# Kernel tuning notes

Hardware: AMD Instinct MI355X
Metric: run time of the kernel (lower is better)

Reference implementation:

```python
import jax, jax.numpy as jnp
import numpy as np

N = 10000      # nodes
E = 320000     # edges (avg degree 32)
D_IN = 128     # input feature dim
D_H = 256      # hidden dim
L = 3          # num GIN layers


def setup_inputs() -> dict:
    key = jax.random.key(0)
    ks = jax.random.split(key, 2 + 4 * L)
    inp = {
        "x": jax.random.normal(ks[0], (N, D_IN), dtype=jnp.float32),
        "edge_index": jax.random.randint(ks[1], (2, E), 0, N, dtype=jnp.int64),
    }
    din = D_IN
    for l in range(L):
        k1, k2, k3, k4 = ks[2 + 4 * l: 6 + 4 * l]
        s1 = 1.0 / np.sqrt(din)
        s2 = 1.0 / np.sqrt(D_H)
        inp[f"w1_{l}"] = jax.random.uniform(k1, (din, D_H), jnp.float32, -s1, s1)
        inp[f"b1_{l}"] = jax.random.uniform(k2, (D_H,), jnp.float32, -s1, s1)
        inp[f"w2_{l}"] = jax.random.uniform(k3, (D_H, D_H), jnp.float32, -s2, s2)
        inp[f"b2_{l}"] = jax.random.uniform(k4, (D_H,), jnp.float32, -s2, s2)
        din = D_H
    return inp


def reference(x, edge_index,
              w1_0, b1_0, w2_0, b2_0,
              w1_1, b1_1, w2_1, b2_1,
              w1_2, b1_2, w2_2, b2_2):
    src, dst = edge_index[0], edge_index[1]
    layers = [(w1_0, b1_0, w2_0, b2_0),
              (w1_1, b1_1, w2_1, b2_1),
              (w1_2, b1_2, w2_2, b2_2)]
    z = x
    for w1, b1, w2, b2 in layers:
        # GINConv with eps=0: h_i = z_i + sum_{j->i} z_j, then 2-layer MLP
        agg = jax.ops.segment_sum(z[src], dst, num_segments=N)  # [N, d]
        h = z + agg
        h = jax.nn.relu(h @ w1 + b1) @ w2 + b2  # nn.Sequential(Linear, ReLU, Linear)
        z = jax.nn.relu(h)                      # Encoder activation
    return z
```

## Files before the change

kernel.cpp:

```cpp
#include <hip/hip_runtime.h>
#include <hip/hip_bf16.h>
#include <cstdint>


#define NNODES 10000
#define NEDGES 320000
#define DIN 128
#define DH 256

typedef __bf16 bf16x8 __attribute__((ext_vector_type(8)));
typedef unsigned short ushort8v __attribute__((ext_vector_type(8)));
typedef unsigned short ushort4v __attribute__((ext_vector_type(4)));
typedef float f32x4 __attribute__((ext_vector_type(4)));

__device__ __forceinline__ unsigned short f2bf(float f) {
    unsigned int u = __float_as_uint(f);
    unsigned int r = u + 0x7fffu + ((u >> 16) & 1u);
    return (unsigned short)(r >> 16);
}
__device__ __forceinline__ float bf2f(unsigned short u) {
    return __uint_as_float(((unsigned int)u) << 16);
}

struct PrepArgs {
    const float* wsrc[6];
    unsigned short* wdst[6];
    int wkbits[6];
    const int* eb;
    int* flag;
    int* cnt;
    const float* x;
    unsigned short* xb;
};
#define PREP_ZERO_B 40
#define PREP_XCONV_B 1250
#define PREP_WCONV_B 352
#define PREP_GRID (PREP_ZERO_B + 1 + PREP_XCONV_B + PREP_WCONV_B)

__global__ void prep_kernel(PrepArgs a) {
    __shared__ float tile[32][33];
    __shared__ int any;
    int bid = blockIdx.x;
    int tid = threadIdx.x;
    if (bid < PREP_ZERO_B) {
        int i = bid * 256 + tid;
        if (i < NNODES) a.cnt[i] = 0;
    } else if (bid == PREP_ZERO_B) {
        if (tid == 0) any = 0;
        __syncthreads();
        for (int i = tid; i < 1024; i += 256)
            if (a.eb[2 * i + 1] != 0) any = 1;
        __syncthreads();
        if (tid == 0) a.flag[0] = any;
    } else if (bid < PREP_ZERO_B + 1 + PREP_XCONV_B) {
        int i = (bid - PREP_ZERO_B - 1) * 256 + tid;
        if (i < NNODES * DIN / 4) {
            float4 v = reinterpret_cast<const float4*>(a.x)[i];
            ushort4v o = {f2bf(v.x), f2bf(v.y), f2bf(v.z), f2bf(v.w)};
            reinterpret_cast<ushort4v*>(a.xb)[i] = o;
        }
    } else {
        int wb = bid - (PREP_ZERO_B + 1 + PREP_XCONV_B);
        int m, t32;
        if (wb < 32) { m = 0; t32 = wb; }
        else { m = 1 + (wb - 32) / 64; t32 = (wb - 32) % 64; }
        int kb = a.wkbits[m];
        int K = 1 << kb;
        int tc = t32 & 7, tr = t32 >> 3;
        int r = tid >> 3, c4 = (tid & 7) * 4;
        float4 v = *reinterpret_cast<const float4*>(
            &a.wsrc[m][(size_t)(tr * 32 + r) * 256 + tc * 32 + c4]);
        tile[r][c4 + 0] = v.x; tile[r][c4 + 1] = v.y;
        tile[r][c4 + 2] = v.z; tile[r][c4 + 3] = v.w;
        __syncthreads();
        int cc = tid >> 3, k4 = (tid & 7) * 4;
        ushort4v o = {f2bf(tile[k4 + 0][cc]), f2bf(tile[k4 + 1][cc]),
                      f2bf(tile[k4 + 2][cc]), f2bf(tile[k4 + 3][cc])};
        *reinterpret_cast<ushort4v*>(
            &a.wdst[m][(size_t)(tc * 32 + cc) * K + tr * 32 + k4]) = o;
    }
}

__device__ __forceinline__ int eload(const int* __restrict__ eb, int is32, long logical_idx) {
    return is32 ? eb[logical_idx] : eb[2 * logical_idx];
}

__global__ void hist_kernel(const int* __restrict__ eb, const int* __restrict__ flag,
                            int* __restrict__ cnt, int E) {
    int i = blockIdx.x * blockDim.x + threadIdx.x;
    if (i >= E) return;
    int is32 = flag[0];
    int d = eload(eb, is32, (long)E + i);
    atomicAdd(&cnt[d], 1);
}

__global__ __launch_bounds__(1024) void scan_kernel(const int* __restrict__ cnt,
                                                    int* __restrict__ offs,
                                                    int* __restrict__ cursor, int n) {
    __shared__ int wsums[16];
    int tid = threadIdx.x, lane = tid & 63, wid = tid >> 6;
    int per = (n + 1023) / 1024;
    int beg = tid * per;
    int local[16];
    int s = 0;
    for (int i = 0; i < per; ++i) {
        int idx = beg + i;
        int v = (idx < n) ? cnt[idx] : 0;
        local[i] = s;
        s += v;
    }
    int inc = s;
    for (int d = 1; d < 64; d <<= 1) {
        int y = __shfl_up(inc, d, 64);
        if (lane >= d) inc += y;
    }
    if (lane == 63) wsums[wid] = inc;
    __syncthreads();
    if (tid < 16) {
        int v = wsums[tid];
        for (int d = 1; d < 16; d <<= 1) {
            int y = __shfl_up(v, d, 64);
            if (tid >= d) v += y;
        }
        wsums[tid] = v;
    }
    __syncthreads();
    int wbase = (wid > 0) ? wsums[wid - 1] : 0;
    int base = wbase + inc - s;
    for (int i = 0; i < per; ++i) {
        int idx = beg + i;
        if (idx < n) {
            int v = base + local[i];
            offs[idx] = v;
            cursor[idx] = v;
        }
    }
    if (tid == 1023) offs[n] = wbase + inc;
}

__global__ void scatter_kernel(const int* __restrict__ eb, const int* __restrict__ flag,
                               int* __restrict__ cursor, int* __restrict__ srcs, int E) {
    int i = blockIdx.x * blockDim.x + threadIdx.x;
    if (i >= E) return;
    int is32 = flag[0];
    int s = eload(eb, is32, (long)i);
    int d = eload(eb, is32, (long)E + i);
    int pos = atomicAdd(&cursor[d], 1);
    srcs[pos] = s;
}

template <int D>
__global__ __launch_bounds__(256) void agg_add_sliced_kernel(const unsigned short* __restrict__ z,
                                                             const int* __restrict__ srcs,
                                                             const int* __restrict__ offs,
                                                             unsigned short* __restrict__ h, int n) {
    constexpr int NSLICE = (D * 2) / 128;
    constexpr int LPN = 8;
    constexpr int NPB = 256 / LPN;
    int bid = blockIdx.x;
    int slice = bid & (NSLICE - 1);
    int ng = bid / NSLICE;
    int t = threadIdx.x;
    int node = ng * NPB + t / LPN;
    if (node >= n) return;
    int li = t % LPN;
    int col8 = slice * LPN + li;
    const ushort8v* zb = reinterpret_cast<const ushort8v*>(z);
    const int ld8 = D / 8;
    int beg = offs[node], end = offs[node + 1];

    float a0[8] = {}, a1[8] = {}, a2[8] = {}, a3[8] = {};
    int e = beg;
    for (; e + 4 <= end; e += 4) {
        int s0 = srcs[e], s1 = srcs[e + 1], s2 = srcs[e + 2], s3 = srcs[e + 3];
        ushort8v v0 = zb[(size_t)s0 * ld8 + col8];
        ushort8v v1 = zb[(size_t)s1 * ld8 + col8];
        ushort8v v2 = zb[(size_t)s2 * ld8 + col8];
        ushort8v v3 = zb[(size_t)s3 * ld8 + col8];
#pragma unroll
        for (int j = 0; j < 8; ++j) {
            a0[j] += bf2f(v0[j]);
            a1[j] += bf2f(v1[j]);
            a2[j] += bf2f(v2[j]);
            a3[j] += bf2f(v3[j]);
        }
    }
    for (; e < end; ++e) {
        ushort8v v = zb[(size_t)srcs[e] * ld8 + col8];
#pragma unroll
        for (int j = 0; j < 8; ++j) a0[j] += bf2f(v[j]);
    }
    ushort8v zr = zb[(size_t)node * ld8 + col8];
    ushort8v o;
#pragma unroll
    for (int j = 0; j < 8; ++j) {
        float v = a0[j] + a1[j] + a2[j] + a3[j] + bf2f(zr[j]);
        o[j] = f2bf(v);
    }
    reinterpret_cast<ushort8v*>(h)[(size_t)node * ld8 + col8] = o;
}

template <int K, int OUT_BF16>
__global__ __launch_bounds__(512) void mlp_fused_kernel(const unsigned short* __restrict__ A,
                                                        const unsigned short* __restrict__ Wt1,
                                                        const float* __restrict__ b1,
                                                        const unsigned short* __restrict__ Wt2,
                                                        const float* __restrict__ b2,
                                                        void* __restrict__ C, int M) {
    constexpr int NK = K / 32;
    constexpr int NST1 = K / 128;
    __shared__ unsigned short As[NK][4][64][8];
    __shared__ unsigned short Bs[4][4][256][8];
    __shared__ unsigned short Ts[8][4][64][8];
    int tid = threadIdx.x;
    int wave = tid >> 6, lane = tid & 63;
    int wr = wave >> 2, wc = wave & 3;
    int m0 = blockIdx.x * 64;
    int fr = lane & 15;
    int kc = lane >> 4;

    f32x4 acc[2][4];
#pragma unroll
    for (int i = 0; i < 2; ++i)
#pragma unroll
        for (int j = 0; j < 4; ++j) acc[i][j] = (f32x4){0.f, 0.f, 0.f, 0.f};

    {
        int row = tid >> 3, c0 = tid & 7;
        int gr = m0 + row;
#pragma unroll
        for (int i = 0; i < K / 64; ++i) {
            int chunk = c0 + i * 8;
            ushort8v av = {0, 0, 0, 0, 0, 0, 0, 0};
            if (gr < M) av = *reinterpret_cast<const ushort8v*>(&A[(size_t)gr * K + chunk * 8]);
            *reinterpret_cast<ushort8v*>(&As[chunk >> 2][chunk & 3][row][0]) = av;
        }
    }
    int scol = tid >> 2;
    int sscn = tid & 3;

#pragma unroll
    for (int st = 0; st < NST1; ++st) {
#pragma unroll
        for (int cp = 0; cp < 2; ++cp) {
            int c = cp * 128 + scol;
#pragma unroll
            for (int kk = 0; kk < 4; ++kk)
                *reinterpret_cast<ushort8v*>(&Bs[kk][sscn][c][0]) =
                    *reinterpret_cast<const ushort8v*>(&Wt1[(size_t)c * K + st * 128 + kk * 32 + sscn * 8]);
        }
        __syncthreads();
#pragma unroll
        for (int kk = 0; kk < 4; ++kk) {
            bf16x8 af[2];
#pragma unroll
            for (int i = 0; i < 2; ++i)
                af[i] = __builtin_bit_cast(bf16x8,
                    *reinterpret_cast<const ushort8v*>(&As[st * 4 + kk][kc][wr * 32 + i * 16 + fr][0]));
#pragma unroll
            for (int j = 0; j < 4; ++j) {
                bf16x8 bf = __builtin_bit_cast(bf16x8,
                    *reinterpret_cast<const ushort8v*>(&Bs[kk][kc][wc * 64 + j * 16 + fr][0]));
#pragma unroll
                for (int i = 0; i < 2; ++i)
                    acc[i][j] = __builtin_amdgcn_mfma_f32_16x16x32_bf16(af[i], bf, acc[i][j], 0, 0, 0);
            }
        }
        __syncthreads();
    }
#pragma unroll
    for (int i = 0; i < 2; ++i)
#pragma unroll
        for (int j = 0; j < 4; ++j) {
            int col = wc * 64 + j * 16 + fr;
            float bb = b1[col];
#pragma unroll
            for (int jj = 0; jj < 4; ++jj) {
                int row = wr * 32 + i * 16 + kc * 4 + jj;
                float v = fmaxf(acc[i][j][jj] + bb, 0.f);
                Ts[col >> 5][(col >> 3) & 3][row][col & 7] = f2bf(v);
            }
            acc[i][j] = (f32x4){0.f, 0.f, 0.f, 0.f};
        }

#pragma unroll
    for (int st = 0; st < 2; ++st) {
#pragma unroll
        for (int cp = 0; cp < 2; ++cp) {
            int c = cp * 128 + scol;
#pragma unroll
            for (int kk = 0; kk < 4; ++kk)
                *reinterpret_cast<ushort8v*>(&Bs[kk][sscn][c][0]) =
                    *reinterpret_cast<const ushort8v*>(&Wt2[(size_t)c * 256 + st * 128 + kk * 32 + sscn * 8]);
        }
        __syncthreads();
#pragma unroll
        for (int kk = 0; kk < 4; ++kk) {
            bf16x8 af[2];
#pragma unroll
            for (int i = 0; i < 2; ++i)
                af[i] = __builtin_bit_cast(bf16x8,
                    *reinterpret_cast<const ushort8v*>(&Ts[st * 4 + kk][kc][wr * 32 + i * 16 + fr][0]));
#pragma unroll
            for (int j = 0; j < 4; ++j) {
                bf16x8 bf = __builtin_bit_cast(bf16x8,
                    *reinterpret_cast<const ushort8v*>(&Bs[kk][kc][wc * 64 + j * 16 + fr][0]));
#pragma unroll
                for (int i = 0; i < 2; ++i)
                    acc[i][j] = __builtin_amdgcn_mfma_f32_16x16x32_bf16(af[i], bf, acc[i][j], 0, 0, 0);
            }
        }
        __syncthreads();
    }
#pragma unroll
    for (int i = 0; i < 2; ++i)
#pragma unroll
        for (int j = 0; j < 4; ++j) {
            int col = wc * 64 + j * 16 + fr;
            float bb = b2[col];
#pragma unroll
            for (int jj = 0; jj < 4; ++jj) {
                int row = m0 + wr * 32 + i * 16 + kc * 4 + jj;
                if (row < M) {
                    float v = fmaxf(acc[i][j][jj] + bb, 0.f);
                    if (OUT_BF16)
                        ((unsigned short*)C)[(size_t)row * 256 + col] = f2bf(v);
                    else
                        ((float*)C)[(size_t)row * 256 + col] = v;
                }
            }
        }
}

extern "C" void kernel_launch(void* const* d_in, const int* in_sizes, int n_in,
                              void* d_out, int out_size, void* d_ws, size_t ws_size,
                              hipStream_t stream) {
    const float* x = (const float*)d_in[0];
    const int* eb = (const int*)d_in[1];
    const int E = NEDGES;
    const int N = NNODES;

    const float* w1[3] = {(const float*)d_in[2], (const float*)d_in[6], (const float*)d_in[10]};
    const float* b1[3] = {(const float*)d_in[3], (const float*)d_in[7], (const float*)d_in[11]};
    const float* w2[3] = {(const float*)d_in[4], (const float*)d_in[8], (const float*)d_in[12]};
    const float* b2[3] = {(const float*)d_in[5], (const float*)d_in[9], (const float*)d_in[13]};

    char* ws = (char*)d_ws;
    size_t off = 0;
    auto alloc = [&](size_t bytes) {
        void* p = ws + off;
        off += (bytes + 255) & ~(size_t)255;
        return p;
    };
    int* flag   = (int*)alloc(4);
    int* cnt    = (int*)alloc((size_t)N * 4);
    int* offs   = (int*)alloc((size_t)(N + 1) * 4);
    int* cursor = (int*)alloc((size_t)N * 4);
    int* srcs   = (int*)alloc((size_t)E * 4);
    unsigned short* xb   = (unsigned short*)alloc((size_t)N * DIN * 2);
    unsigned short* zbuf = (unsigned short*)alloc((size_t)N * DH * 2);
    unsigned short* hbuf = (unsigned short*)alloc((size_t)N * DH * 2);
    unsigned short* wt[6];
    wt[0] = (unsigned short*)alloc((size_t)DIN * DH * 2);
    for (int i = 1; i < 6; ++i) wt[i] = (unsigned short*)alloc((size_t)DH * DH * 2);
    (void)ws_size; (void)n_in; (void)out_size; (void)in_sizes;

    PrepArgs pa;
    pa.wsrc[0] = w1[0]; pa.wsrc[1] = w2[0]; pa.wsrc[2] = w1[1];
    pa.wsrc[3] = w2[1]; pa.wsrc[4] = w1[2]; pa.wsrc[5] = w2[2];
    for (int i = 0; i < 6; ++i) pa.wdst[i] = wt[i];
    pa.wkbits[0] = 7;
    for (int i = 1; i < 6; ++i) pa.wkbits[i] = 8;
    pa.eb = eb; pa.flag = flag; pa.cnt = cnt; pa.x = x; pa.xb = xb;
    prep_kernel<<<PREP_GRID, 256, 0, stream>>>(pa);

    hist_kernel<<<(E + 255) / 256, 256, 0, stream>>>(eb, flag, cnt, E);
    scan_kernel<<<1, 1024, 0, stream>>>(cnt, offs, cursor, N);
    scatter_kernel<<<(E + 255) / 256, 256, 0, stream>>>(eb, flag, cursor, srcs, E);

    int mlp_grid = (N + 63) / 64;
    int agg_blocks_256 = ((N + 31) / 32) * 4;
    int agg_blocks_128 = ((N + 31) / 32) * 2;

    agg_add_sliced_kernel<128><<<agg_blocks_128, 256, 0, stream>>>(xb, srcs, offs, hbuf, N);
    mlp_fused_kernel<128, 1><<<mlp_grid, 512, 0, stream>>>(hbuf, wt[0], b1[0], wt[1], b2[0], zbuf, N);

    agg_add_sliced_kernel<256><<<agg_blocks_256, 256, 0, stream>>>(zbuf, srcs, offs, hbuf, N);
    mlp_fused_kernel<256, 1><<<mlp_grid, 512, 0, stream>>>(hbuf, wt[2], b1[1], wt[3], b2[1], zbuf, N);

    agg_add_sliced_kernel<256><<<agg_blocks_256, 256, 0, stream>>>(zbuf, srcs, offs, hbuf, N);
    mlp_fused_kernel<256, 0><<<mlp_grid, 512, 0, stream>>>(hbuf, wt[4], b1[2], wt[5], b2[2], (float*)d_out, N);
}
```

Baseline: 146.7 us.

## Prefetch next weight tile into registers while computing current stage in fused MLP

Restructures the fused two-layer MLP kernel so the next 128-wide weight slab is loaded from global memory into registers while MFMAs run on the current slab in shared memory. Each register slab is written to shared memory after a barrier. This software pipelining is meant to hide global weight-load latency behind compute. It costs 8 extra 16-byte vector registers per thread, which may affect occupancy, and it adds a more intricate barrier schedule.

New measurement: 146.7 us. Within noise of the previous version (-0.0%).

```diff
diff --git a/kernel.cpp b/kernel.cpp
--- a/kernel.cpp
+++ b/kernel.cpp
@@ -218,6 +218,8 @@
     int m0 = blockIdx.x * 64;
     int fr = lane & 15;
     int kc = lane >> 4;
+    int scol = tid >> 2;
+    int sscn = tid & 3;
 
     f32x4 acc[2][4];
 #pragma unroll
@@ -225,6 +227,83 @@
 #pragma unroll
         for (int j = 0; j < 4; ++j) acc[i][j] = (f32x4){0.f, 0.f, 0.f, 0.f};
 
+    ushort8v wreg[8];
+#define LOAD_W(Wp, ldk, st)                                                   \
+    {                                                                         \
+        _Pragma("unroll")                                                     \
+        for (int cp = 0; cp < 2; ++cp) {                                      \
+            _Pragma("unroll")                                                 \
+            for (int kk = 0; kk < 4; ++kk)                                    \
+                wreg[cp * 4 + kk] = *reinterpret_cast<const ushort8v*>(       \
+                    &(Wp)[(size_t)(cp * 128 + scol) * (ldk) + (st) * 128 +    \
+                          kk * 32 + sscn * 8]);                               \
+        }                                                                     \
+    }
+#define WRITE_W()                                                             \
+    {                                                                         \
+        _Pragma("unroll")                                                     \
+        for (int cp = 0; cp < 2; ++cp) {                                      \
+            _Pragma("unroll")                                                 \
+            for (int kk = 0; kk < 4; ++kk)                                    \
+                *reinterpret_cast<ushort8v*>(                                 \
+                    &Bs[kk][sscn][cp * 128 + scol][0]) = wreg[cp * 4 + kk];   \
+        }                                                                     \
+    }
+
+    auto compute_p1 = [&](int st) {
+#pragma unroll
+        for (int kk = 0; kk < 4; ++kk) {
+            bf16x8 af[2];
+#pragma unroll
+            for (int i = 0; i < 2; ++i)
+                af[i] = __builtin_bit_cast(bf16x8,
+                    *reinterpret_cast<const ushort8v*>(&As[st * 4 + kk][kc][wr * 32 + i * 16 + fr][0]));
+#pragma unroll
+            for (int j = 0; j < 4; ++j) {
+                bf16x8 bf = __builtin_bit_cast(bf16x8,
+                    *reinterpret_cast<const ushort8v*>(&Bs[kk][kc][wc * 64 + j * 16 + fr][0]));
+#pragma unroll
+                for (int i = 0; i < 2; ++i)
+                    acc[i][j] = __builtin_amdgcn_mfma_f32_16x16x32_bf16(af[i], bf, acc[i][j], 0, 0, 0);
+            }
+        }
+    };
+    auto compute_p2 = [&](int st) {
+#pragma unroll
+        for (int kk = 0; kk < 4; ++kk) {
+            bf16x8 af[2];
+#pragma unroll
+            for (int i = 0; i < 2; ++i)
+                af[i] = __builtin_bit_cast(bf16x8,
+                    *reinterpret_cast<const ushort8v*>(&Ts[st * 4 + kk][kc][wr * 32 + i * 16 + fr][0]));
+#pragma unroll
+            for (int j = 0; j < 4; ++j) {
+                bf16x8 bf = __builtin_bit_cast(bf16x8,
+                    *reinterpret_cast<const ushort8v*>(&Bs[kk][kc][wc * 64 + j * 16 + fr][0]));
+#pragma unroll
+                for (int i = 0; i < 2; ++i)
+                    acc[i][j] = __builtin_amdgcn_mfma_f32_16x16x32_bf16(af[i], bf, acc[i][j], 0, 0, 0);
+            }
+        }
+    };
+    auto epilogue1 = [&]() {
+#pragma unroll
+        for (int i = 0; i < 2; ++i)
+#pragma unroll
+            for (int j = 0; j < 4; ++j) {
+                int col = wc * 64 + j * 16 + fr;
+                float bb = b1[col];
+#pragma unroll
+                for (int jj = 0; jj < 4; ++jj) {
+                    int row = wr * 32 + i * 16 + kc * 4 + jj;
+                    float v = fmaxf(acc[i][j][jj] + bb, 0.f);
+                    Ts[col >> 5][(col >> 3) & 3][row][col & 7] = f2bf(v);
+                }
+                acc[i][j] = (f32x4){0.f, 0.f, 0.f, 0.f};
+            }
+    };
+
+    LOAD_W(Wt1, K, 0);
     {
         int row = tid >> 3, c0 = tid & 7;
         int gr = m0 + row;
@@ -236,82 +315,29 @@
             *reinterpret_cast<ushort8v*>(&As[chunk >> 2][chunk & 3][row][0]) = av;
         }
     }
-    int scol = tid >> 2;
-    int sscn = tid & 3;
-
-#pragma unroll
-    for (int st = 0; st < NST1; ++st) {
-#pragma unroll
-        for (int cp = 0; cp < 2; ++cp) {
-            int c = cp * 128 + scol;
-#pragma unroll
-            for (int kk = 0; kk < 4; ++kk)
-                *reinterpret_cast<ushort8v*>(&Bs[kk][sscn][c][0]) =
-                    *reinterpret_cast<const ushort8v*>(&Wt1[(size_t)c * K + st * 128 + kk * 32 + sscn * 8]);
-        }
+    WRITE_W();
+    if (NST1 > 1) { LOAD_W(Wt1, K, 1); } else { LOAD_W(Wt2, 256, 0); }
+    __syncthreads();
+    compute_p1(0);
+    if (NST1 == 1) epilogue1();
+    __syncthreads();
+    WRITE_W();
+    if (NST1 > 1) { LOAD_W(Wt2, 256, 0); } else { LOAD_W(Wt2, 256, 1); }
+    __syncthreads();
+    if (NST1 > 1) {
+        compute_p1(1);
+        epilogue1();
         __syncthreads();
-#pragma unroll
-        for (int kk = 0; kk < 4; ++kk) {
-            bf16x8 af[2];
-#pragma unroll
-            for (int i = 0; i < 2; ++i)
-                af[i] = __builtin_bit_cast(bf16x8,
-                    *reinterpret_cast<const ushort8v*>(&As[st * 4 + kk][kc][wr * 32 + i * 16 + fr][0]));
-#pragma unroll
-            for (int j = 0; j < 4; ++j) {
-                bf16x8 bf = __builtin_bit_cast(bf16x8,
-                    *reinterpret_cast<const ushort8v*>(&Bs[kk][kc][wc * 64 + j * 16 + fr][0]));
-#pragma unroll
-                for (int i = 0; i < 2; ++i)
-                    acc[i][j] = __builtin_amdgcn_mfma_f32_16x16x32_bf16(af[i], bf, acc[i][j], 0, 0, 0);
-            }
-        }
+        WRITE_W();
+        LOAD_W(Wt2, 256, 1);
         __syncthreads();
     }
-#pragma unroll
-    for (int i = 0; i < 2; ++i)
-#pragma unroll
-        for (int j = 0; j < 4; ++j) {
-            int col = wc * 64 + j * 16 + fr;
-            float bb = b1[col];
-#pragma unroll
-            for (int jj = 0; jj < 4; ++jj) {
-                int row = wr * 32 + i * 16 + kc * 4 + jj;
-                float v = fmaxf(acc[i][j][jj] + bb, 0.f);
-                Ts[col >> 5][(col >> 3) & 3][row][col & 7] = f2bf(v);
-            }
-            acc[i][j] = (f32x4){0.f, 0.f, 0.f, 0.f};
-        }
-
-#pragma unroll
-    for (int st = 0; st < 2; ++st) {
-#pragma unroll
-        for (int cp = 0; cp < 2; ++cp) {
-            int c = cp * 128 + scol;
-#pragma unroll
-            for (int kk = 0; kk < 4; ++kk)
-                *reinterpret_cast<ushort8v*>(&Bs[kk][sscn][c][0]) =
-                    *reinterpret_cast<const ushort8v*>(&Wt2[(size_t)c * 256 + st * 128 + kk * 32 + sscn * 8]);
-        }
-        __syncthreads();
-#pragma unroll
-        for (int kk = 0; kk < 4; ++kk) {
-            bf16x8 af[2];
-#pragma unroll
-            for (int i = 0; i < 2; ++i)
-                af[i] = __builtin_bit_cast(bf16x8,
-                    *reinterpret_cast<const ushort8v*>(&Ts[st * 4 + kk][kc][wr * 32 + i * 16 + fr][0]));
-#pragma unroll
-            for (int j = 0; j < 4; ++j) {
-                bf16x8 bf = __builtin_bit_cast(bf16x8,
-                    *reinterpret_cast<const ushort8v*>(&Bs[kk][kc][wc * 64 + j * 16 + fr][0]));
-#pragma unroll
-                for (int i = 0; i < 2; ++i)
-                    acc[i][j] = __builtin_amdgcn_mfma_f32_16x16x32_bf16(af[i], bf, acc[i][j], 0, 0, 0);
-            }
-        }
-        __syncthreads();
-    }
+    compute_p2(0);
+    __syncthreads();
+    WRITE_W();
+    __syncthreads();
+    compute_p2(1);
+
 #pragma unroll
     for (int i = 0; i < 2; ++i)
 #pragma unroll
@@ -330,6 +356,8 @@
                 }
             }
         }
+#undef LOAD_W
+#undef WRITE_W
 }
 
 extern "C" void kernel_launch(void* const* d_in, const int* in_sizes, int n_in,
```

## Split fused MLP into separate 64x64-tiled GEMMs and prefetch edge indices

Applied to the files above, without the earlier changes.

Replaces the fused two-GEMM MLP kernel, which used one 512-thread block per 64 rows, with a standalone GEMM kernel tiled 64x64 over a 2D grid. Each MLP layer now runs as two launches with an intermediate bf16 buffer, giving four times as many blocks for better CU occupancy. The cost is an extra global round trip for the hidden activations and more kernel launches. The aggregation loop also software-prefetches the next four source indices so gather addresses are ready earlier.

Result: slower. 173.4 us (+18.1%).

```diff
diff --git a/kernel.cpp b/kernel.cpp
--- a/kernel.cpp
+++ b/kernel.cpp
@@ -171,18 +171,29 @@
 
     float a0[8] = {}, a1[8] = {}, a2[8] = {}, a3[8] = {};
     int e = beg;
-    for (; e + 4 <= end; e += 4) {
+    if (e + 4 <= end) {
         int s0 = srcs[e], s1 = srcs[e + 1], s2 = srcs[e + 2], s3 = srcs[e + 3];
-        ushort8v v0 = zb[(size_t)s0 * ld8 + col8];
-        ushort8v v1 = zb[(size_t)s1 * ld8 + col8];
-        ushort8v v2 = zb[(size_t)s2 * ld8 + col8];
-        ushort8v v3 = zb[(size_t)s3 * ld8 + col8];
-#pragma unroll
-        for (int j = 0; j < 8; ++j) {
-            a0[j] += bf2f(v0[j]);
-            a1[j] += bf2f(v1[j]);
-            a2[j] += bf2f(v2[j]);
-            a3[j] += bf2f(v3[j]);
+        while (true) {
+            int n0 = 0, n1 = 0, n2 = 0, n3 = 0;
+            bool more = (e + 8 <= end);
+            if (more) {
+                n0 = srcs[e + 4]; n1 = srcs[e + 5];
+                n2 = srcs[e + 6]; n3 = srcs[e + 7];
+            }
+            ushort8v v0 = zb[(size_t)s0 * ld8 + col8];
+            ushort8v v1 = zb[(size_t)s1 * ld8 + col8];
+            ushort8v v2 = zb[(size_t)s2 * ld8 + col8];
+            ushort8v v3 = zb[(size_t)s3 * ld8 + col8];
+#pragma unroll
+            for (int j = 0; j < 8; ++j) {
+                a0[j] += bf2f(v0[j]);
+                a1[j] += bf2f(v1[j]);
+                a2[j] += bf2f(v2[j]);
+                a3[j] += bf2f(v3[j]);
+            }
+            e += 4;
+            if (!more) break;
+            s0 = n0; s1 = n1; s2 = n2; s3 = n3;
         }
     }
     for (; e < end; ++e) {
@@ -201,123 +212,66 @@
 }
 
 template <int K, int OUT_BF16>
-__global__ __launch_bounds__(512) void mlp_fused_kernel(const unsigned short* __restrict__ A,
-                                                        const unsigned short* __restrict__ Wt1,
-                                                        const float* __restrict__ b1,
-                                                        const unsigned short* __restrict__ Wt2,
-                                                        const float* __restrict__ b2,
-                                                        void* __restrict__ C, int M) {
+__global__ __launch_bounds__(256) void gemm_kernel(const unsigned short* __restrict__ A,
+                                                   const unsigned short* __restrict__ Wt,
+                                                   const float* __restrict__ bias,
+                                                   void* __restrict__ C, int M) {
     constexpr int NK = K / 32;
-    constexpr int NST1 = K / 128;
     __shared__ unsigned short As[NK][4][64][8];
-    __shared__ unsigned short Bs[4][4][256][8];
-    __shared__ unsigned short Ts[8][4][64][8];
+    __shared__ unsigned short Bs[NK][4][64][8];
     int tid = threadIdx.x;
     int wave = tid >> 6, lane = tid & 63;
-    int wr = wave >> 2, wc = wave & 3;
+    int wr = wave >> 1, wc = wave & 1;
     int m0 = blockIdx.x * 64;
+    int n0 = blockIdx.y * 64;
     int fr = lane & 15;
     int kc = lane >> 4;
 
-    f32x4 acc[2][4];
+    f32x4 acc[2][2];
 #pragma unroll
     for (int i = 0; i < 2; ++i)
 #pragma unroll
-        for (int j = 0; j < 4; ++j) acc[i][j] = (f32x4){0.f, 0.f, 0.f, 0.f};
+        for (int j = 0; j < 2; ++j) acc[i][j] = (f32x4){0.f, 0.f, 0.f, 0.f};
 
     {
-        int row = tid >> 3, c0 = tid & 7;
+        int row = tid >> 2, c0 = tid & 3;
         int gr = m0 + row;
 #pragma unroll
-        for (int i = 0; i < K / 64; ++i) {
-            int chunk = c0 + i * 8;
+        for (int i = 0; i < K / 32; ++i) {
+            int chunk = c0 + i * 4;
             ushort8v av = {0, 0, 0, 0, 0, 0, 0, 0};
             if (gr < M) av = *reinterpret_cast<const ushort8v*>(&A[(size_t)gr * K + chunk * 8]);
             *reinterpret_cast<ushort8v*>(&As[chunk >> 2][chunk & 3][row][0]) = av;
-        }
-    }
-    int scol = tid >> 2;
-    int sscn = tid & 3;
-
-#pragma unroll
-    for (int st = 0; st < NST1; ++st) {
-#pragma unroll
-        for (int cp = 0; cp < 2; ++cp) {
-            int c = cp * 128 + scol;
-#pragma unroll
-            for (int kk = 0; kk < 4; ++kk)
-                *reinterpret_cast<ushort8v*>(&Bs[kk][sscn][c][0]) =
-                    *reinterpret_cast<const ushort8v*>(&Wt1[(size_t)c * K + st * 128 + kk * 32 + sscn * 8]);
-        }
-        __syncthreads();
-#pragma unroll
-        for (int kk = 0; kk < 4; ++kk) {
-            bf16x8 af[2];
-#pragma unroll
-            for (int i = 0; i < 2; ++i)
-                af[i] = __builtin_bit_cast(bf16x8,
-                    *reinterpret_cast<const ushort8v*>(&As[st * 4 + kk][kc][wr * 32 + i * 16 + fr][0]));
-#pragma unroll
-            for (int j = 0; j < 4; ++j) {
-                bf16x8 bf = __builtin_bit_cast(bf16x8,
-                    *reinterpret_cast<const ushort8v*>(&Bs[kk][kc][wc * 64 + j * 16 + fr][0]));
-#pragma unroll
-                for (int i = 0; i < 2; ++i)
-                    acc[i][j] = __builtin_amdgcn_mfma_f32_16x16x32_bf16(af[i], bf, acc[i][j], 0, 0, 0);
-            }
-        }
-        __syncthreads();
-    }
+            ushort8v bv = *reinterpret_cast<const ushort8v*>(&Wt[(size_t)(n0 + row) * K + chunk * 8]);
+            *reinterpret_cast<ushort8v*>(&Bs[chunk >> 2][chunk & 3][row][0]) = bv;
+        }
+    }
+    __syncthreads();
+
+#pragma unroll
+    for (int kk = 0; kk < NK; ++kk) {
+        bf16x8 af[2], bf[2];
+#pragma unroll
+        for (int i = 0; i < 2; ++i)
+            af[i] = __builtin_bit_cast(bf16x8,
+                *reinterpret_cast<const ushort8v*>(&As[kk][kc][wr * 32 + i * 16 + fr][0]));
+#pragma unroll
+        for (int j = 0; j < 2; ++j)
+            bf[j] = __builtin_bit_cast(bf16x8,
+                *reinterpret_cast<const ushort8v*>(&Bs[kk][kc][wc * 32 + j * 16 + fr][0]));
+#pragma unroll
+        for (int i = 0; i < 2; ++i)
+#pragma unroll
+            for (int j = 0; j < 2; ++j)
+                acc[i][j] = __builtin_amdgcn_mfma_f32_16x16x32_bf16(af[i], bf[j], acc[i][j], 0, 0, 0);
+    }
+
 #pragma unroll
     for (int i = 0; i < 2; ++i)
 #pragma unroll
-        for (int j = 0; j < 4; ++j) {
-            int col = wc * 64 + j * 16 + fr;
-            float bb = b1[col];
-#pragma unroll
-            for (int jj = 0; jj < 4; ++jj) {
-                int row = wr * 32 + i * 16 + kc * 4 + jj;
-                float v = fmaxf(acc[i][j][jj] + bb, 0.f);
-                Ts[col >> 5][(col >> 3) & 3][row][col & 7] = f2bf(v);
-            }
-            acc[i][j] = (f32x4){0.f, 0.f, 0.f, 0.f};
-        }
-
-#pragma unroll
-    for (int st = 0; st < 2; ++st) {
-#pragma unroll
-        for (int cp = 0; cp < 2; ++cp) {
-            int c = cp * 128 + scol;
-#pragma unroll
-            for (int kk = 0; kk < 4; ++kk)
-                *reinterpret_cast<ushort8v*>(&Bs[kk][sscn][c][0]) =
-                    *reinterpret_cast<const ushort8v*>(&Wt2[(size_t)c * 256 + st * 128 + kk * 32 + sscn * 8]);
-        }
-        __syncthreads();
-#pragma unroll
-        for (int kk = 0; kk < 4; ++kk) {
-            bf16x8 af[2];
-#pragma unroll
-            for (int i = 0; i < 2; ++i)
-                af[i] = __builtin_bit_cast(bf16x8,
-                    *reinterpret_cast<const ushort8v*>(&Ts[st * 4 + kk][kc][wr * 32 + i * 16 + fr][0]));
-#pragma unroll
-            for (int j = 0; j < 4; ++j) {
-                bf16x8 bf = __builtin_bit_cast(bf16x8,
-                    *reinterpret_cast<const ushort8v*>(&Bs[kk][kc][wc * 64 + j * 16 + fr][0]));
-#pragma unroll
-                for (int i = 0; i < 2; ++i)
-                    acc[i][j] = __builtin_amdgcn_mfma_f32_16x16x32_bf16(af[i], bf, acc[i][j], 0, 0, 0);
-            }
-        }
-        __syncthreads();
-    }
-#pragma unroll
-    for (int i = 0; i < 2; ++i)
-#pragma unroll
-        for (int j = 0; j < 4; ++j) {
-            int col = wc * 64 + j * 16 + fr;
-            float bb = b2[col];
+        for (int j = 0; j < 2; ++j) {
+            int col = n0 + wc * 32 + j * 16 + fr;
+            float bb = bias[col];
 #pragma unroll
             for (int jj = 0; jj < 4; ++jj) {
                 int row = m0 + wr * 32 + i * 16 + kc * 4 + jj;
@@ -360,6 +314,7 @@
     unsigned short* xb   = (unsigned short*)alloc((size_t)N * DIN * 2);
     unsigned short* zbuf = (unsigned short*)alloc((size_t)N * DH * 2);
     unsigned short* hbuf = (unsigned short*)alloc((size_t)N * DH * 2);
+    unsigned short* tbuf = (unsigned short*)alloc((size_t)N * DH * 2);
     unsigned short* wt[6];
     wt[0] = (unsigned short*)alloc((size_t)DIN * DH * 2);
     for (int i = 1; i < 6; ++i) wt[i] = (unsigned short*)alloc((size_t)DH * DH * 2);
@@ -378,16 +333,19 @@
     scan_kernel<<<1, 1024, 0, stream>>>(cnt, offs, cursor, N);
     scatter_kernel<<<(E + 255) / 256, 256, 0, stream>>>(eb, flag, cursor, srcs, E);
 
-    int mlp_grid = (N + 63) / 64;
+    dim3 gemm_grid((N + 63) / 64, 4);
     int agg_blocks_256 = ((N + 31) / 32) * 4;
     int agg_blocks_128 = ((N + 31) / 32) * 2;
 
     agg_add_sliced_kernel<128><<<agg_blocks_128, 256, 0, stream>>>(xb, srcs, offs, hbuf, N);
-    mlp_fused_kernel<128, 1><<<mlp_grid, 512, 0, stream>>>(hbuf, wt[0], b1[0], wt[1], b2[0], zbuf, N);
+    gemm_kernel<128, 1><<<gemm_grid, 256, 0, stream>>>(hbuf, wt[0], b1[0], tbuf, N);
+    gemm_kernel<256, 1><<<gemm_grid, 256, 0, stream>>>(tbuf, wt[1], b2[0], zbuf, N);
 
     agg_add_sliced_kernel<256><<<agg_blocks_256, 256, 0, stream>>>(zbuf, srcs, offs, hbuf, N);
-    mlp_fused_kernel<256, 1><<<mlp_grid, 512, 0, stream>>>(hbuf, wt[2], b1[1], wt[3], b2[1], zbuf, N);
+    gemm_kernel<256, 1><<<gemm_grid, 256, 0, stream>>>(hbuf, wt[2], b1[1], tbuf, N);
+    gemm_kernel<256, 1><<<gemm_grid, 256, 0, stream>>>(tbuf, wt[3], b2[1], zbuf, N);
 
     agg_add_sliced_kernel<256><<<agg_blocks_256, 256, 0, stream>>>(zbuf, srcs, offs, hbuf, N);
-    mlp_fused_kernel<256, 0><<<mlp_grid, 512, 0, stream>>>(hbuf, wt[4], b1[2], wt[5], b2[2], (float*)d_out, N);
-}
+    gemm_kernel<256, 1><<<gemm_grid, 256, 0, stream>>>(hbuf, wt[4], b1[2], tbuf, N);
+    gemm_kernel<256, 0><<<gemm_grid, 256, 0, stream>>>(tbuf, wt[5], b2[2], (float*)d_out, N);
+}
```
